# Kernel tuning notes

Measured on AMD Instinct MI355X. Metric: run time of the kernel, lower is better.

The kernel has to match this reference:

```python
import jax, jax.numpy as jnp
import numpy as np

N, P, D, C = 8192, 512, 2, 4   # queries, coeff grid points, spatial dim, num coefficients
HA = 32                        # attention_net hidden
HP, CP = 32, 16                # pointswise_mlp hidden / output
HG = 256                       # green_function_net hidden


def setup_inputs() -> dict:
    key = jax.random.key(0)
    ks = jax.random.split(key, 16)
    g = lambda k, shp, s: jax.random.normal(k, shp, dtype=jnp.float32) * s
    return {
        "r": g(ks[0], (N, 2 * D), 1.0),
        "r_prime": g(ks[1], (N, 2 * D), 1.0),
        "coeff_x": g(ks[2], (P, D), 1.0),
        "coeff_y": g(ks[3], (P, C), 1.0),
        # attention_net MLP (no bias): concat(q,k)=4 -> 32 -> 32 -> 1
        "Wa1": g(ks[4], (2 * D, HA), 0.5),
        "Wa2": g(ks[5], (HA, HA), 1.0 / np.sqrt(HA)),
        "Wa3": g(ks[6], (HA, 1), 1.0 / np.sqrt(HA)),
        # pointswise_mlp: C -> 32 -> 16
        "Wp1": g(ks[7], (C, HP), 0.5), "bp1": jnp.zeros((HP,), jnp.float32),
        "Wp2": g(ks[8], (HP, CP), 1.0 / np.sqrt(HP)), "bp2": jnp.zeros((CP,), jnp.float32),
        # green_function_net: 4+4+16=24 -> 256 -> 256 -> 1 (exp at the end)
        "Wg1": g(ks[9], (2 * D + 2 * D + CP, HG), 1.0 / np.sqrt(24.0)), "bg1": jnp.zeros((HG,), jnp.float32),
        "Wg2": g(ks[10], (HG, HG), 1.0 / np.sqrt(HG)), "bg2": jnp.zeros((HG,), jnp.float32),
        "Wg3": g(ks[11], (HG, 1), 0.1 / np.sqrt(HG)), "bg3": jnp.zeros((1,), jnp.float32),
    }


def reference(r, r_prime, coeff_x, coeff_y,
              Wa1, Wa2, Wa3, Wp1, bp1, Wp2, bp2,
              Wg1, bg1, Wg2, bg2, Wg3, bg3):
    # --- CoefficientNet: pairwise MLP attention over the coefficient grid ---
    q = r[:, :D]  # (N, 2) spatial position only
    # first layer of attn MLP on concat([q, k]) split into q- and k- parts
    h = jax.nn.relu(q @ Wa1[:D][None if False else slice(None)]  # (N, HA)
                    [..., :] [..., :]  # no-op for readability
                    if False else (q @ Wa1[:D])[:, None, :] + (coeff_x @ Wa1[D:])[None, :, :])  # (N, P, HA)
    h = jax.nn.relu(h @ Wa2)                     # (N, P, HA)
    logits = (h @ Wa3)[..., 0]                   # (N, P)
    attn = jax.nn.softmax(logits, axis=-1)       # (N, P)
    attn_out = attn @ coeff_y                    # (N, C)
    c = jax.nn.relu(attn_out @ Wp1 + bp1) @ Wp2 + bp2  # (N, CP)
    # --- GreenFunctionNet ---
    x = jnp.concatenate([r, r_prime, c], axis=-1)       # (N, 24)
    g1 = jax.nn.relu(x @ Wg1 + bg1)
    g2 = jax.nn.relu(g1 @ Wg2 + bg2)
    return jnp.exp(g2 @ Wg3 + bg3)                      # (N, 1)
```

## Files before the change

### kernel.cpp

```cpp
#include <hip/hip_runtime.h>
#include <math.h>

#define N_ 8192
#define P_ 512

typedef __fp16 half8  __attribute__((ext_vector_type(8)));
typedef __fp16 half2t __attribute__((ext_vector_type(2)));
typedef float  floatx16 __attribute__((ext_vector_type(16)));

union H8 { half8 v; half2t h2[4]; };

static __device__ __forceinline__ half2t pk2(float a, float b) {
    return __builtin_amdgcn_cvt_pkrtz(a, b);
}

#define HP_OFF 17408
#define XS_OFF 21760

__global__ __launch_bounds__(512, 4) void k_fused(
    const float* __restrict__ r,
    const float* __restrict__ rp,
    const float* __restrict__ coeff_x,
    const float* __restrict__ coeff_y,
    const float* __restrict__ Wa1,
    const float* __restrict__ Wa2,
    const float* __restrict__ Wa3,
    const float* __restrict__ Wp1,
    const float* __restrict__ bp1,
    const float* __restrict__ Wp2,
    const float* __restrict__ bp2,
    const float* __restrict__ Wg1,
    const float* __restrict__ bg1,
    const float* __restrict__ Wg2,
    const float* __restrict__ bg2,
    const float* __restrict__ Wg3,
    const float* __restrict__ bg3,
    float* __restrict__ out)
{
    __shared__ __align__(16) unsigned char reg0[49152];
    __shared__ __align__(16) float4 cyS[512];
    __shared__ float sA[8][32];
    __shared__ float aoA[4][8][32];
    __shared__ float aoS[32][4];

    const int tid  = threadIdx.x;
    const int n0   = blockIdx.x * 32;
    const int lane = tid & 63;
    const int wv   = tid >> 6;
    const int j32  = lane & 31;
    const int hl   = lane >> 5;
    const int k0g  = hl * 8;

    {
        const float2 cx = ((const float2*)coeff_x)[tid];
        half2t* wrow = (half2t*)(reg0 + tid * 96);
#pragma unroll
        for (int q = 0; q < 16; ++q) {
            const float b0 = cx.x * Wa1[64 + 2*q]     + cx.y * Wa1[96 + 2*q];
            const float b1 = cx.x * Wa1[64 + 2*q + 1] + cx.y * Wa1[96 + 2*q + 1];
            wrow[q] = pk2(b0, b1);
        }
        cyS[tid] = ((const float4*)coeff_y)[tid];
    }

    H8 anh1, anh2;
    {
        const float2 rv = ((const float2*)r)[2 * (n0 + j32)];
#pragma unroll
        for (int q = 0; q < 4; ++q) {
            const int k1 = k0g + 2*q, k2 = 16 + k0g + 2*q;
            anh1.h2[q] = pk2(rv.x*Wa1[k1]   + rv.y*Wa1[32+k1],
                             rv.x*Wa1[k1+1] + rv.y*Wa1[32+k1+1]);
            anh2.h2[q] = pk2(rv.x*Wa1[k2]   + rv.y*Wa1[32+k2],
                             rv.x*Wa1[k2+1] + rv.y*Wa1[32+k2+1]);
        }
    }
    H8 af1, af2;
#pragma unroll
    for (int q = 0; q < 4; ++q) {
        af1.h2[q] = pk2(Wa2[(k0g + 2*q)     * 32 + j32],
                        Wa2[(k0g + 2*q + 1) * 32 + j32]);
        af2.h2[q] = pk2(Wa2[(16 + k0g + 2*q)     * 32 + j32],
                        Wa2[(16 + k0g + 2*q + 1) * 32 + j32]);
    }
    half2t w3h[8];
#pragma unroll
    for (int q = 0; q < 8; ++q) {
        const int r0 = ((2*q) & 3) + 8*(q >> 1) + 4*hl;
        w3h[q] = pk2(Wa3[r0], Wa3[r0 + 1]);
    }

    __syncthreads();

    const half2t zero2 = pk2(0.f, 0.f);
    float s = 0.0f, aox = 0.f, aoy = 0.f, aoz = 0.f, aow = 0.f;

#pragma unroll 2
    for (int pl = 0; pl < 64; ++pl) {
        const int ploc = wv * 64 + pl;
        const half2t* rowq = (const half2t*)(reg0 + ploc * 96) + hl * 4;

        H8 bf1, bf2;
#pragma unroll
        for (int q = 0; q < 4; ++q) {
            bf1.h2[q] = __builtin_elementwise_max(anh1.h2[q] + rowq[q],     zero2);
            bf2.h2[q] = __builtin_elementwise_max(anh2.h2[q] + rowq[8 + q], zero2);
        }

        floatx16 zc = {};
        floatx16 acc = __builtin_amdgcn_mfma_f32_32x32x16_f16(af1.v, bf1.v, zc, 0, 0, 0);
        acc = __builtin_amdgcn_mfma_f32_32x32x16_f16(af2.v, bf2.v, acc, 0, 0, 0);

        float d0, d1, d2, d3;
        {
            half2t z0 = __builtin_elementwise_max(pk2(acc[0],  acc[1]),  zero2);
            half2t z1 = __builtin_elementwise_max(pk2(acc[2],  acc[3]),  zero2);
            half2t z2 = __builtin_elementwise_max(pk2(acc[4],  acc[5]),  zero2);
            half2t z3 = __builtin_elementwise_max(pk2(acc[6],  acc[7]),  zero2);
            half2t z4 = __builtin_elementwise_max(pk2(acc[8],  acc[9]),  zero2);
            half2t z5 = __builtin_elementwise_max(pk2(acc[10], acc[11]), zero2);
            half2t z6 = __builtin_elementwise_max(pk2(acc[12], acc[13]), zero2);
            half2t z7 = __builtin_elementwise_max(pk2(acc[14], acc[15]), zero2);
            d0 = __builtin_amdgcn_fdot2(z1, w3h[1], __builtin_amdgcn_fdot2(z0, w3h[0], 0.f, false), false);
            d1 = __builtin_amdgcn_fdot2(z3, w3h[3], __builtin_amdgcn_fdot2(z2, w3h[2], 0.f, false), false);
            d2 = __builtin_amdgcn_fdot2(z5, w3h[5], __builtin_amdgcn_fdot2(z4, w3h[4], 0.f, false), false);
            d3 = __builtin_amdgcn_fdot2(z7, w3h[7], __builtin_amdgcn_fdot2(z6, w3h[6], 0.f, false), false);
        }
        float dot = (d0 + d1) + (d2 + d3);
        dot += __shfl_xor(dot, 32);

        const float e = __expf(dot);
        const float4 cyv = cyS[ploc];
        s   += e;
        aox += e * cyv.x;
        aoy += e * cyv.y;
        aoz += e * cyv.z;
        aow += e * cyv.w;
    }

    if (lane < 32) {
        sA[wv][lane]      = s;
        aoA[0][wv][lane]  = aox;
        aoA[1][wv][lane]  = aoy;
        aoA[2][wv][lane]  = aoz;
        aoA[3][wv][lane]  = aow;
    }
    __syncthreads();

    if (tid < 32) {
        float S = 0.f, A0 = 0.f, A1 = 0.f, A2 = 0.f, A3 = 0.f;
#pragma unroll
        for (int w = 0; w < 8; ++w) {
            S  += sA[w][tid];
            A0 += aoA[0][w][tid];
            A1 += aoA[1][w][tid];
            A2 += aoA[2][w][tid];
            A3 += aoA[3][w][tid];
        }
        const float inv = 1.0f / S;
        aoS[tid][0] = A0 * inv;
        aoS[tid][1] = A1 * inv;
        aoS[tid][2] = A2 * inv;
        aoS[tid][3] = A3 * inv;
    }
    __syncthreads();

    float* hpS = (float*)(reg0 + HP_OFF);
    float* xS  = (float*)(reg0 + XS_OFF);
    const int nB = tid & 31;
    const int iB = tid >> 5;

    if (tid < 256) {
        const int nn = tid >> 3, k = tid & 7;
        xS[nn*25 + k] = (k < 4) ? r[(n0+nn)*4 + k] : rp[(n0+nn)*4 + k - 4];
    }
    {
        const float a0 = aoS[nB][0], a1 = aoS[nB][1], a2 = aoS[nB][2], a3 = aoS[nB][3];
#pragma unroll
        for (int rep = 0; rep < 2; ++rep) {
            const int i = iB + rep*16;
            float a = bp1[i] + a0*Wp1[i] + a1*Wp1[32+i] + a2*Wp1[64+i] + a3*Wp1[96+i];
            hpS[nB*33 + i] = fmaxf(a, 0.0f);
        }
    }
    __syncthreads();

    {
        float a = bp2[iB];
#pragma unroll
        for (int i = 0; i < 32; ++i) a += hpS[nB*33 + i] * Wp2[i*16 + iB];
        xS[nB*25 + 8 + iB] = a;
    }
    __syncthreads();

    const int jcol = (wv << 5) + j32;
    __fp16* g1S = (__fp16*)reg0;

    {
        H8 xa1, xa2, wb1, wb2;
        const float* xrow = xS + j32 * 25;
#pragma unroll
        for (int q = 0; q < 4; ++q) {
            xa1.h2[q] = pk2(xrow[k0g + 2*q], xrow[k0g + 2*q + 1]);
            wb1.h2[q] = pk2(Wg1[(k0g + 2*q)*256 + jcol],
                            Wg1[(k0g + 2*q + 1)*256 + jcol]);
            if (hl == 0) {
                xa2.h2[q] = pk2(xrow[16 + 2*q], xrow[16 + 2*q + 1]);
                wb2.h2[q] = pk2(Wg1[(16 + 2*q)*256 + jcol],
                                Wg1[(17 + 2*q)*256 + jcol]);
            } else {
                xa2.h2[q] = pk2(0.f, 0.f);
                wb2.h2[q] = pk2(0.f, 0.f);
            }
        }
        floatx16 g1acc = {};
        g1acc = __builtin_amdgcn_mfma_f32_32x32x16_f16(xa1.v, wb1.v, g1acc, 0, 0, 0);
        g1acc = __builtin_amdgcn_mfma_f32_32x32x16_f16(xa2.v, wb2.v, g1acc, 0, 0, 0);

        const float b1v = bg1[jcol];
#pragma unroll
        for (int i = 0; i < 16; ++i) {
            const int row = (i & 3) + 8*(i >> 2) + 4*hl;
            g1S[row*264 + jcol] = (__fp16)fmaxf(g1acc[i] + b1v, 0.0f);
        }
    }
    __syncthreads();

    {
        floatx16 acc2 = {};
        const __fp16* arow = g1S + j32 * 264;

        H8 wB[4], wBn[4];
#pragma unroll
        for (int q = 0; q < 4; ++q) {
            const int kb = q*16 + hl*8;
#pragma unroll
            for (int t = 0; t < 4; ++t)
                wB[q].h2[t] = pk2(Wg2[(kb + 2*t)*256 + jcol],
                                  Wg2[(kb + 2*t + 1)*256 + jcol]);
        }
#pragma unroll
        for (int c = 0; c < 4; ++c) {
            if (c < 3) {
#pragma unroll
                for (int q = 0; q < 4; ++q) {
                    const int kb = (c*4 + 4 + q)*16 + hl*8;
#pragma unroll
                    for (int t = 0; t < 4; ++t)
                        wBn[q].h2[t] = pk2(Wg2[(kb + 2*t)*256 + jcol],
                                           Wg2[(kb + 2*t + 1)*256 + jcol]);
                }
            }
#pragma unroll
            for (int q = 0; q < 4; ++q) {
                H8 af;
                af.v = *(const half8*)(arow + (c*4 + q)*16 + hl*8);
                acc2 = __builtin_amdgcn_mfma_f32_32x32x16_f16(af.v, wB[q].v, acc2, 0, 0, 0);
            }
#pragma unroll
            for (int q = 0; q < 4; ++q) wB[q] = wBn[q];
        }

        const float b2v = bg2[jcol];
        const float w3v = Wg3[jcol];
        float part[16];
#pragma unroll
        for (int i = 0; i < 16; ++i)
            part[i] = fmaxf(acc2[i] + b2v, 0.0f) * w3v;
#pragma unroll
        for (int off = 1; off <= 16; off <<= 1) {
#pragma unroll
            for (int i = 0; i < 16; ++i) part[i] += __shfl_xor(part[i], off);
        }
        float* redS = &sA[0][0];
        if ((lane & 31) == 0) {
#pragma unroll
            for (int i = 0; i < 16; ++i) {
                const int row = (i & 3) + 8*(i >> 2) + 4*hl;
                redS[wv*32 + row] = part[i];
            }
        }
        __syncthreads();

        if (tid < 32) {
            float v = bg3[0];
#pragma unroll
            for (int w = 0; w < 8; ++w) v += redS[w*32 + tid];
            out[n0 + tid] = __expf(v);
        }
    }
}

extern "C" void kernel_launch(void* const* d_in, const int* in_sizes, int n_in,
                              void* d_out, int out_size, void* d_ws, size_t ws_size,
                              hipStream_t stream)
{
    const float* r   = (const float*)d_in[0];
    const float* rp  = (const float*)d_in[1];
    const float* cx  = (const float*)d_in[2];
    const float* cy  = (const float*)d_in[3];
    const float* Wa1 = (const float*)d_in[4];
    const float* Wa2 = (const float*)d_in[5];
    const float* Wa3 = (const float*)d_in[6];
    const float* Wp1 = (const float*)d_in[7];
    const float* bp1 = (const float*)d_in[8];
    const float* Wp2 = (const float*)d_in[9];
    const float* bp2 = (const float*)d_in[10];
    const float* Wg1 = (const float*)d_in[11];
    const float* bg1 = (const float*)d_in[12];
    const float* Wg2 = (const float*)d_in[13];
    const float* bg2 = (const float*)d_in[14];
    const float* Wg3 = (const float*)d_in[15];
    const float* bg3 = (const float*)d_in[16];

    hipLaunchKernelGGL(k_fused, dim3(N_/32), dim3(512), 0, stream,
                       r, rp, cx, cy, Wa1, Wa2, Wa3, Wp1, bp1, Wp2, bp2,
                       Wg1, bg1, Wg2, bg2, Wg3, bg3, (float*)d_out);
}
```

Measured before the change: 111.7 us.

## Double block size to 1024 threads and split-K the green-net second layer

```diff
diff --git a/kernel.cpp b/kernel.cpp
--- a/kernel.cpp
+++ b/kernel.cpp
@@ -14,10 +14,12 @@
     return __builtin_amdgcn_cvt_pkrtz(a, b);
 }
 
-#define HP_OFF 17408
-#define XS_OFF 21760
-
-__global__ __launch_bounds__(512, 4) void k_fused(
+#define HP_OFF  17408
+#define XS_OFF  21760
+#define ACC_OFF 25088
+#define REG0_SZ 57856
+
+__global__ __launch_bounds__(1024, 4) void k_fused(
     const float* __restrict__ r,
     const float* __restrict__ rp,
     const float* __restrict__ coeff_x,
@@ -37,10 +39,10 @@
     const float* __restrict__ bg3,
     float* __restrict__ out)
 {
-    __shared__ __align__(16) unsigned char reg0[49152];
+    __shared__ __align__(16) unsigned char reg0[REG0_SZ];
     __shared__ __align__(16) float4 cyS[512];
-    __shared__ float sA[8][32];
-    __shared__ float aoA[4][8][32];
+    __shared__ float sA[16][32];
+    __shared__ float aoA[4][16][32];
     __shared__ float aoS[32][4];
 
     const int tid  = threadIdx.x;
@@ -51,7 +53,7 @@
     const int hl   = lane >> 5;
     const int k0g  = hl * 8;
 
-    {
+    if (tid < 512) {
         const float2 cx = ((const float2*)coeff_x)[tid];
         half2t* wrow = (half2t*)(reg0 + tid * 96);
 #pragma unroll
@@ -96,8 +98,8 @@
     float s = 0.0f, aox = 0.f, aoy = 0.f, aoz = 0.f, aow = 0.f;
 
 #pragma unroll 2
-    for (int pl = 0; pl < 64; ++pl) {
-        const int ploc = wv * 64 + pl;
+    for (int pl = 0; pl < 32; ++pl) {
+        const int ploc = wv * 32 + pl;
         const half2t* rowq = (const half2t*)(reg0 + ploc * 96) + hl * 4;
 
         H8 bf1, bf2;
@@ -150,7 +152,7 @@
     if (tid < 32) {
         float S = 0.f, A0 = 0.f, A1 = 0.f, A2 = 0.f, A3 = 0.f;
 #pragma unroll
-        for (int w = 0; w < 8; ++w) {
+        for (int w = 0; w < 16; ++w) {
             S  += sA[w][tid];
             A0 += aoA[0][w][tid];
             A1 += aoA[1][w][tid];
@@ -176,27 +178,24 @@
     }
     {
         const float a0 = aoS[nB][0], a1 = aoS[nB][1], a2 = aoS[nB][2], a3 = aoS[nB][3];
-#pragma unroll
-        for (int rep = 0; rep < 2; ++rep) {
-            const int i = iB + rep*16;
-            float a = bp1[i] + a0*Wp1[i] + a1*Wp1[32+i] + a2*Wp1[64+i] + a3*Wp1[96+i];
-            hpS[nB*33 + i] = fmaxf(a, 0.0f);
-        }
-    }
-    __syncthreads();
-
-    {
-        float a = bp2[iB];
-#pragma unroll
-        for (int i = 0; i < 32; ++i) a += hpS[nB*33 + i] * Wp2[i*16 + iB];
-        xS[nB*25 + 8 + iB] = a;
-    }
-    __syncthreads();
-
-    const int jcol = (wv << 5) + j32;
+        float a = bp1[iB] + a0*Wp1[iB] + a1*Wp1[32+iB] + a2*Wp1[64+iB] + a3*Wp1[96+iB];
+        hpS[nB*33 + iB] = fmaxf(a, 0.0f);
+    }
+    __syncthreads();
+
+    if (tid < 512) {
+        const int i2 = tid >> 5;
+        float a = bp2[i2];
+#pragma unroll
+        for (int i = 0; i < 32; ++i) a += hpS[nB*33 + i] * Wp2[i*16 + i2];
+        xS[nB*25 + 8 + i2] = a;
+    }
+    __syncthreads();
+
     __fp16* g1S = (__fp16*)reg0;
 
-    {
+    if (wv < 8) {
+        const int jcol = (wv << 5) + j32;
         H8 xa1, xa2, wb1, wb2;
         const float* xrow = xS + j32 * 25;
 #pragma unroll
@@ -227,57 +226,76 @@
     __syncthreads();
 
     {
+        const int g   = wv >> 3;
+        const int wv8 = wv & 7;
+        const int jc  = (wv8 << 5) + j32;
+        const int B0  = g << 7;
+        float* accS = (float*)(reg0 + ACC_OFF);
+        float* redS = &sA[0][0];
+
         floatx16 acc2 = {};
-        const __fp16* arow = g1S + j32 * 264;
+        const __fp16* arow = g1S + j32 * 264 + B0;
 
         H8 wB[4], wBn[4];
 #pragma unroll
         for (int q = 0; q < 4; ++q) {
-            const int kb = q*16 + hl*8;
+            const int kb = B0 + q*16 + hl*8;
 #pragma unroll
             for (int t = 0; t < 4; ++t)
-                wB[q].h2[t] = pk2(Wg2[(kb + 2*t)*256 + jcol],
-                                  Wg2[(kb + 2*t + 1)*256 + jcol]);
-        }
-#pragma unroll
-        for (int c = 0; c < 4; ++c) {
-            if (c < 3) {
+                wB[q].h2[t] = pk2(Wg2[(kb + 2*t)*256 + jc],
+                                  Wg2[(kb + 2*t + 1)*256 + jc]);
+        }
+#pragma unroll
+        for (int c = 0; c < 2; ++c) {
+            if (c == 0) {
 #pragma unroll
                 for (int q = 0; q < 4; ++q) {
-                    const int kb = (c*4 + 4 + q)*16 + hl*8;
+                    const int kb = B0 + 64 + q*16 + hl*8;
 #pragma unroll
                     for (int t = 0; t < 4; ++t)
-                        wBn[q].h2[t] = pk2(Wg2[(kb + 2*t)*256 + jcol],
-                                           Wg2[(kb + 2*t + 1)*256 + jcol]);
+                        wBn[q].h2[t] = pk2(Wg2[(kb + 2*t)*256 + jc],
+                                           Wg2[(kb + 2*t + 1)*256 + jc]);
                 }
             }
 #pragma unroll
             for (int q = 0; q < 4; ++q) {
                 H8 af;
-                af.v = *(const half8*)(arow + (c*4 + q)*16 + hl*8);
+                af.v = *(const half8*)(arow + c*64 + q*16 + hl*8);
                 acc2 = __builtin_amdgcn_mfma_f32_32x32x16_f16(af.v, wB[q].v, acc2, 0, 0, 0);
             }
 #pragma unroll
             for (int q = 0; q < 4; ++q) wB[q] = wBn[q];
         }
 
-        const float b2v = bg2[jcol];
-        const float w3v = Wg3[jcol];
-        float part[16];
-#pragma unroll
-        for (int i = 0; i < 16; ++i)
-            part[i] = fmaxf(acc2[i] + b2v, 0.0f) * w3v;
-#pragma unroll
-        for (int off = 1; off <= 16; off <<= 1) {
-#pragma unroll
-            for (int i = 0; i < 16; ++i) part[i] += __shfl_xor(part[i], off);
-        }
-        float* redS = &sA[0][0];
-        if ((lane & 31) == 0) {
+        if (g == 1) {
 #pragma unroll
             for (int i = 0; i < 16; ++i) {
                 const int row = (i & 3) + 8*(i >> 2) + 4*hl;
-                redS[wv*32 + row] = part[i];
+                accS[row*256 + jc] = acc2[i];
+            }
+        }
+        __syncthreads();
+
+        if (g == 0) {
+            const float b2v = bg2[jc];
+            const float w3v = Wg3[jc];
+            float part[16];
+#pragma unroll
+            for (int i = 0; i < 16; ++i) {
+                const int row = (i & 3) + 8*(i >> 2) + 4*hl;
+                part[i] = fmaxf(acc2[i] + accS[row*256 + jc] + b2v, 0.0f) * w3v;
+            }
+#pragma unroll
+            for (int off = 1; off <= 16; off <<= 1) {
+#pragma unroll
+                for (int i = 0; i < 16; ++i) part[i] += __shfl_xor(part[i], off);
+            }
+            if ((lane & 31) == 0) {
+#pragma unroll
+                for (int i = 0; i < 16; ++i) {
+                    const int row = (i & 3) + 8*(i >> 2) + 4*hl;
+                    redS[wv8*32 + row] = part[i];
+                }
             }
         }
         __syncthreads();
@@ -313,7 +331,7 @@
     const float* Wg3 = (const float*)d_in[15];
     const float* bg3 = (const float*)d_in[16];
 
-    hipLaunchKernelGGL(k_fused, dim3(N_/32), dim3(512), 0, stream,
+    hipLaunchKernelGGL(k_fused, dim3(N_/32), dim3(1024), 0, stream,
                        r, rp, cx, cy, Wa1, Wa2, Wa3, Wp1, bp1, Wp2, bp2,
                        Wg1, bg1, Wg2, bg2, Wg3, bg3, (float*)d_out);
 }
```

Measured after the change: 112.9 us. Within noise of the previous version (+1.0%).
